# Performance work log

Hardware: AMD Instinct MI355X
Metric: run time of the kernel (lower is better)

Reference implementation:

```python
import jax, jax.numpy as jnp
import numpy as np

N = 100000
E = 3200000
IN_DIM = 128
HID = 64
BN_EPS = 1e-5


def _gcn_conv(x, W, b, src, dst, dinv):
    h = x @ W                                      # [N, out]
    coeff = (dinv[src] * dinv[dst])[:, None]       # [E, 1]
    msg = h[src] * coeff                           # gather over edges
    agg = jax.ops.segment_sum(msg, dst, num_segments=N)
    agg = agg + h * (dinv * dinv)[:, None]         # self-loop term
    return agg + b


def setup_inputs() -> dict:
    key = jax.random.key(0)
    ks = jax.random.split(key, 12)
    x = jax.random.normal(ks[0], (N, IN_DIM), dtype=jnp.float32)
    edge_index = jax.random.randint(ks[1], (2, E), 0, N, dtype=jnp.int64)
    s1 = 1.0 / np.sqrt(IN_DIM)
    s2 = 1.0 / np.sqrt(HID)
    W1 = jax.random.uniform(ks[2], (IN_DIM, HID), jnp.float32, -s1, s1)
    b1 = jnp.zeros((HID,), jnp.float32)
    W2 = jax.random.uniform(ks[3], (HID, HID), jnp.float32, -s2, s2)
    b2 = jnp.zeros((HID,), jnp.float32)
    W3 = jax.random.uniform(ks[4], (HID, 1), jnp.float32, -s2, s2)
    b3 = jnp.zeros((1,), jnp.float32)
    g1 = jnp.ones((HID,), jnp.float32)
    beta1 = jnp.zeros((HID,), jnp.float32)
    m1 = 0.1 * jax.random.normal(ks[5], (HID,), jnp.float32)
    v1 = jax.random.uniform(ks[6], (HID,), jnp.float32) + 0.5
    g2 = jnp.ones((HID,), jnp.float32)
    beta2 = jnp.zeros((HID,), jnp.float32)
    m2 = 0.1 * jax.random.normal(ks[7], (HID,), jnp.float32)
    v2 = jax.random.uniform(ks[8], (HID,), jnp.float32) + 0.5
    return {"x": x, "edge_index": edge_index,
            "W1": W1, "b1": b1, "W2": W2, "b2": b2, "W3": W3, "b3": b3,
            "g1": g1, "beta1": beta1, "m1": m1, "v1": v1,
            "g2": g2, "beta2": beta2, "m2": m2, "v2": v2}


def reference(x, edge_index, W1, b1, W2, b2, W3, b3,
              g1, beta1, m1, v1, g2, beta2, m2, v2):
    src, dst = edge_index[0], edge_index[1]
    # degree with self-loops (computed on destination index, PyG convention)
    deg = jax.ops.segment_sum(jnp.ones((E,), jnp.float32), dst, num_segments=N) + 1.0
    dinv = jax.lax.rsqrt(deg)

    def bn(h, g, beta, m, v):
        return (h - m) * jax.lax.rsqrt(v + BN_EPS) * g + beta

    h = _gcn_conv(x, W1, b1, src, dst, dinv)
    h = jax.nn.relu(bn(h, g1, beta1, m1, v1))  # dropout is a no-op in eval
    h = _gcn_conv(h, W2, b2, src, dst, dinv)
    h = jax.nn.relu(bn(h, g2, beta2, m2, v2))
    h = _gcn_conv(h, W3, b3, src, dst, dinv)
    return jax.nn.sigmoid(h)  # [N, 1]
```

## Files before the change

kernel.cpp:

```cpp
#include <hip/hip_runtime.h>
#include <math.h>

#define N_NODES 100000
#define E_EDGES 3200000
#define IN_DIM_ 128
#define HID_ 64
#define BN_EPS_ 1e-5f

#define PB 200
#define CHUNK 16000
#define NBUCK 391

typedef __attribute__((ext_vector_type(8))) short short8;
typedef __attribute__((ext_vector_type(4))) float f32x4;

__device__ inline ushort f2bf(float f) {
    union { float f; unsigned u; } c; c.f = f;
    unsigned r = c.u + 0x7fff + ((c.u >> 16) & 1);
    return (ushort)(r >> 16);
}
__device__ inline float bf_lo(unsigned p) { union { unsigned u; float f; } c; c.u = p << 16; return c.f; }
__device__ inline float bf_hi(unsigned p) { union { unsigned u; float f; } c; c.u = p & 0xffff0000u; return c.f; }

__global__ __launch_bounds__(256) void passA1_hist(const int* __restrict__ ei,
                                                   int* __restrict__ histPB) {
    __shared__ int hist[NBUCK];
    int t = threadIdx.x, b = blockIdx.x;
    for (int k = t; k < NBUCK; k += 256) hist[k] = 0;
    __syncthreads();
    int e0 = b * CHUNK, e1 = e0 + CHUNK;
    for (int e = e0 + t; e < e1; e += 256) {
        int d = ei[E_EDGES + e];
        atomicAdd(&hist[d >> 8], 1);
    }
    __syncthreads();
    for (int k = t; k < NBUCK; k += 256) histPB[k * PB + b] = hist[k];
}

__global__ __launch_bounds__(256) void scan_rows(int* __restrict__ histPB,
                                                 int* __restrict__ bucket_tot) {
    __shared__ int wsum[4];
    int k = blockIdx.x, t = threadIdx.x, lane = t & 63, wv = t >> 6;
    int v = (t < PB) ? histPB[k * PB + t] : 0;
    int s = v;
#pragma unroll
    for (int off = 1; off < 64; off <<= 1) {
        int u = __shfl_up(s, off, 64);
        if (lane >= off) s += u;
    }
    if (lane == 63) wsum[wv] = s;
    __syncthreads();
    int wbase = 0;
    for (int w = 0; w < wv; w++) wbase += wsum[w];
    if (t < PB) histPB[k * PB + t] = wbase + s - v;
    if (t == 255) bucket_tot[k] = wbase + s;
}

__global__ __launch_bounds__(512) void scan_totals(const int* __restrict__ bucket_tot,
                                                   int* __restrict__ bucket_base,
                                                   int* __restrict__ row_ptr) {
    __shared__ int wsum[8];
    int t = threadIdx.x, lane = t & 63, wv = t >> 6;
    int v = (t < NBUCK) ? bucket_tot[t] : 0;
    int s = v;
#pragma unroll
    for (int off = 1; off < 64; off <<= 1) {
        int u = __shfl_up(s, off, 64);
        if (lane >= off) s += u;
    }
    if (lane == 63) wsum[wv] = s;
    __syncthreads();
    int wbase = 0;
    for (int w = 0; w < wv; w++) wbase += wsum[w];
    if (t < NBUCK) bucket_base[t] = wbase + s - v;
    if (t == 0) {
        bucket_base[NBUCK] = E_EDGES;
        row_ptr[N_NODES] = E_EDGES;
    }
}

__global__ __launch_bounds__(256) void passA2_scatter(const int* __restrict__ ei,
                                                      const int* __restrict__ histPB,
                                                      const int* __restrict__ bucket_base,
                                                      int* __restrict__ ebuf) {
    __shared__ int cur[NBUCK];
    int t = threadIdx.x, b = blockIdx.x;
    for (int k = t; k < NBUCK; k += 256) cur[k] = bucket_base[k] + histPB[k * PB + b];
    __syncthreads();
    int e0 = b * CHUNK, e1 = e0 + CHUNK;
    for (int e = e0 + t; e < e1; e += 256) {
        int s = ei[e];
        int d = ei[E_EDGES + e];
        int bk = d >> 8;
        int pos = atomicAdd(&cur[bk], 1);
        ebuf[pos] = s | ((d & 255) << 17);
    }
}

__global__ __launch_bounds__(256) void passB_place(const int* __restrict__ ebuf,
                                                   const int* __restrict__ bucket_base,
                                                   int* __restrict__ row_ptr,
                                                   int* __restrict__ csr_src,
                                                   float* __restrict__ dinv) {
    __shared__ int hist[256];
    __shared__ int wsum[4];
    int b = blockIdx.x, t = threadIdx.x, lane = t & 63, wv = t >> 6;
    int base = bucket_base[b], end = bucket_base[b + 1];
    hist[t] = 0;
    __syncthreads();
    for (int k = base + t; k < end; k += 256)
        atomicAdd(&hist[ebuf[k] >> 17], 1);
    __syncthreads();
    int v = hist[t];
    int s = v;
#pragma unroll
    for (int off = 1; off < 64; off <<= 1) {
        int u = __shfl_up(s, off, 64);
        if (lane >= off) s += u;
    }
    if (lane == 63) wsum[wv] = s;
    __syncthreads();
    int wbase = 0;
    for (int w = 0; w < wv; w++) wbase += wsum[w];
    int excl = wbase + s - v;
    int node = b * 256 + t;
    if (node < N_NODES) {
        row_ptr[node] = base + excl;
        dinv[node] = rsqrtf((float)v + 1.0f);
    }
    __syncthreads();
    hist[t] = excl;
    __syncthreads();
    for (int k = base + t; k < end; k += 256) {
        int pv = ebuf[k];
        int pos = atomicAdd(&hist[pv >> 17], 1);
        csr_src[base + pos] = pv & 0x1FFFF;
    }
}

template<int K, bool BF16IN>
__global__ __launch_bounds__(256) void gemm_bf16(const void* __restrict__ Xv,
                                                 const float* __restrict__ W,
                                                 const float* __restrict__ dinv,
                                                 ushort* __restrict__ hs) {
    constexpr int KP = K + 8;
    __shared__ ushort A_lds[64][KP];
    __shared__ ushort Wt_lds[64][KP];
    int t = threadIdx.x;
    long row0 = (long)blockIdx.x * 64;

    for (int i = t; i < K * 16; i += 256) {
        float4 w4 = ((const float4*)W)[i];
        int k = i >> 4, n = (i & 15) * 4;
        Wt_lds[n + 0][k] = f2bf(w4.x);
        Wt_lds[n + 1][k] = f2bf(w4.y);
        Wt_lds[n + 2][k] = f2bf(w4.z);
        Wt_lds[n + 3][k] = f2bf(w4.w);
    }
    if (BF16IN) {
        constexpr int K2 = K / 2;
        const unsigned* X = (const unsigned*)Xv;
        for (int i = t; i < 64 * K2; i += 256) {
            int r = i / K2, c = i % K2;
            unsigned val = 0;
            long row = row0 + r;
            if (row < N_NODES) val = X[row * K2 + c];
            *(unsigned*)&A_lds[r][c * 2] = val;
        }
    } else {
        constexpr int K4 = K / 4;
        const float* X = (const float*)Xv;
        for (int i = t; i < 64 * K4; i += 256) {
            int r = i / K4, c = i % K4;
            float4 val = make_float4(0.f, 0.f, 0.f, 0.f);
            long row = row0 + r;
            if (row < N_NODES) val = ((const float4*)X)[row * K4 + c];
            int cb = c * 4;
            A_lds[r][cb + 0] = f2bf(val.x);
            A_lds[r][cb + 1] = f2bf(val.y);
            A_lds[r][cb + 2] = f2bf(val.z);
            A_lds[r][cb + 3] = f2bf(val.w);
        }
    }
    __syncthreads();

    int w = t >> 6, l = t & 63;
    int m = l & 15, quad = l >> 4;
    f32x4 acc[4];
#pragma unroll
    for (int c = 0; c < 4; c++) acc[c] = (f32x4){0.f, 0.f, 0.f, 0.f};

#pragma unroll
    for (int ch = 0; ch < K / 32; ch++) {
        short8 a = *(const short8*)&A_lds[16 * w + m][32 * ch + 8 * quad];
#pragma unroll
        for (int c = 0; c < 4; c++) {
            short8 b = *(const short8*)&Wt_lds[16 * c + m][32 * ch + 8 * quad];
            acc[c] = __builtin_amdgcn_mfma_f32_16x16x32_bf16(a, b, acc[c], 0, 0, 0);
        }
    }

#pragma unroll
    for (int r = 0; r < 4; r++) {
        long node = row0 + 16 * w + quad * 4 + r;
        if (node < N_NODES) {
            float dv = dinv[node];
#pragma unroll
            for (int c = 0; c < 4; c++)
                hs[node * 64 + 16 * c + m] = f2bf(acc[c][r] * dv);
        }
    }
}

template<bool LAST>
__global__ __launch_bounds__(256) void gather_feat(const int* __restrict__ row_ptr,
                                                   const int* __restrict__ csr_src,
                                                   const ushort* __restrict__ hs,
                                                   const float* __restrict__ dinv,
                                                   const float* __restrict__ b,
                                                   const float* __restrict__ g,
                                                   const float* __restrict__ beta,
                                                   const float* __restrict__ m,
                                                   const float* __restrict__ v,
                                                   unsigned* __restrict__ y,
                                                   const float* __restrict__ W3,
                                                   float* __restrict__ hs3, int n) {
    int i = (blockIdx.x * 256 + threadIdx.x) >> 6;
    if (i >= n) return;
    int l = threadIdx.x & 63;
    int es = l >> 3, fg = l & 7;
    const uint4* H4 = (const uint4*)hs;

    float a0 = 0.f, a1 = 0.f, a2 = 0.f, a3 = 0.f;
    float a4 = 0.f, a5 = 0.f, a6 = 0.f, a7 = 0.f;

    if (es == 0) {
        uint4 p = H4[(long)i * 8 + fg];
        a0 += bf_lo(p.x); a1 += bf_hi(p.x);
        a2 += bf_lo(p.y); a3 += bf_hi(p.y);
        a4 += bf_lo(p.z); a5 += bf_hi(p.z);
        a6 += bf_lo(p.w); a7 += bf_hi(p.w);
    }

    int beg = row_ptr[i], end = row_ptr[i + 1];
    int k = beg;
    for (; k + 16 <= end; k += 16) {
        int sA = csr_src[k + es];
        int sB = csr_src[k + 8 + es];
        uint4 pA = H4[(long)sA * 8 + fg];
        uint4 pB = H4[(long)sB * 8 + fg];
        a0 += bf_lo(pA.x) + bf_lo(pB.x); a1 += bf_hi(pA.x) + bf_hi(pB.x);
        a2 += bf_lo(pA.y) + bf_lo(pB.y); a3 += bf_hi(pA.y) + bf_hi(pB.y);
        a4 += bf_lo(pA.z) + bf_lo(pB.z); a5 += bf_hi(pA.z) + bf_hi(pB.z);
        a6 += bf_lo(pA.w) + bf_lo(pB.w); a7 += bf_hi(pA.w) + bf_hi(pB.w);
    }
    for (; k + 8 <= end; k += 8) {
        int s = csr_src[k + es];
        uint4 p = H4[(long)s * 8 + fg];
        a0 += bf_lo(p.x); a1 += bf_hi(p.x);
        a2 += bf_lo(p.y); a3 += bf_hi(p.y);
        a4 += bf_lo(p.z); a5 += bf_hi(p.z);
        a6 += bf_lo(p.w); a7 += bf_hi(p.w);
    }
    int rem = end - k;
    if (es < rem) {
        int s = csr_src[k + es];
        uint4 p = H4[(long)s * 8 + fg];
        a0 += bf_lo(p.x); a1 += bf_hi(p.x);
        a2 += bf_lo(p.y); a3 += bf_hi(p.y);
        a4 += bf_lo(p.z); a5 += bf_hi(p.z);
        a6 += bf_lo(p.w); a7 += bf_hi(p.w);
    }

#pragma unroll
    for (int off = 8; off < 64; off <<= 1) {
        a0 += __shfl_xor(a0, off, 64);
        a1 += __shfl_xor(a1, off, 64);
        a2 += __shfl_xor(a2, off, 64);
        a3 += __shfl_xor(a3, off, 64);
        a4 += __shfl_xor(a4, off, 64);
        a5 += __shfl_xor(a5, off, 64);
        a6 += __shfl_xor(a6, off, 64);
        a7 += __shfl_xor(a7, off, 64);
    }

    float4 bb0 = ((const float4*)b)[fg * 2],    bb1 = ((const float4*)b)[fg * 2 + 1];
    float4 gg0 = ((const float4*)g)[fg * 2],    gg1 = ((const float4*)g)[fg * 2 + 1];
    float4 be0 = ((const float4*)beta)[fg * 2], be1 = ((const float4*)beta)[fg * 2 + 1];
    float4 mm0 = ((const float4*)m)[fg * 2],    mm1 = ((const float4*)m)[fg * 2 + 1];
    float4 vv0 = ((const float4*)v)[fg * 2],    vv1 = ((const float4*)v)[fg * 2 + 1];
    float di = dinv[i];
    float o0 = fmaxf((di * a0 + bb0.x - mm0.x) * (gg0.x * rsqrtf(vv0.x + BN_EPS_)) + be0.x, 0.f);
    float o1 = fmaxf((di * a1 + bb0.y - mm0.y) * (gg0.y * rsqrtf(vv0.y + BN_EPS_)) + be0.y, 0.f);
    float o2 = fmaxf((di * a2 + bb0.z - mm0.z) * (gg0.z * rsqrtf(vv0.z + BN_EPS_)) + be0.z, 0.f);
    float o3 = fmaxf((di * a3 + bb0.w - mm0.w) * (gg0.w * rsqrtf(vv0.w + BN_EPS_)) + be0.w, 0.f);
    float o4 = fmaxf((di * a4 + bb1.x - mm1.x) * (gg1.x * rsqrtf(vv1.x + BN_EPS_)) + be1.x, 0.f);
    float o5 = fmaxf((di * a5 + bb1.y - mm1.y) * (gg1.y * rsqrtf(vv1.y + BN_EPS_)) + be1.y, 0.f);
    float o6 = fmaxf((di * a6 + bb1.z - mm1.z) * (gg1.z * rsqrtf(vv1.z + BN_EPS_)) + be1.z, 0.f);
    float o7 = fmaxf((di * a7 + bb1.w - mm1.w) * (gg1.w * rsqrtf(vv1.w + BN_EPS_)) + be1.w, 0.f);

    if (LAST) {
        float4 w30 = ((const float4*)W3)[fg * 2], w31 = ((const float4*)W3)[fg * 2 + 1];
        float p = o0 * w30.x + o1 * w30.y + o2 * w30.z + o3 * w30.w +
                  o4 * w31.x + o5 * w31.y + o6 * w31.z + o7 * w31.w;
#pragma unroll
        for (int off = 1; off < 8; off <<= 1)
            p += __shfl_xor(p, off, 64);
        if (l == 0) hs3[i] = p * di;
    } else {
        if (es == 0) {
            uint4 pk;
            pk.x = (unsigned)f2bf(o0) | ((unsigned)f2bf(o1) << 16);
            pk.y = (unsigned)f2bf(o2) | ((unsigned)f2bf(o3) << 16);
            pk.z = (unsigned)f2bf(o4) | ((unsigned)f2bf(o5) << 16);
            pk.w = (unsigned)f2bf(o6) | ((unsigned)f2bf(o7) << 16);
            ((uint4*)y)[(long)i * 8 + fg] = pk;
        }
    }
}

__global__ __launch_bounds__(256) void gather3(const int* __restrict__ row_ptr,
                                               const int* __restrict__ csr_src,
                                               const float* __restrict__ hs3,
                                               const float* __restrict__ dinv,
                                               const float* __restrict__ b3,
                                               float* __restrict__ out, int n) {
    int i = blockIdx.x * 256 + threadIdx.x;
    if (i >= n) return;
    int beg = row_ptr[i], end = row_ptr[i + 1];
    float s0 = hs3[i], s1 = 0.f, s2 = 0.f, s3 = 0.f;
    float s4 = 0.f, s5 = 0.f, s6 = 0.f, s7 = 0.f;
    int k = beg;
    for (; k + 8 <= end; k += 8) {
        s0 += hs3[csr_src[k]];
        s1 += hs3[csr_src[k + 1]];
        s2 += hs3[csr_src[k + 2]];
        s3 += hs3[csr_src[k + 3]];
        s4 += hs3[csr_src[k + 4]];
        s5 += hs3[csr_src[k + 5]];
        s6 += hs3[csr_src[k + 6]];
        s7 += hs3[csr_src[k + 7]];
    }
    for (; k < end; k++) s0 += hs3[csr_src[k]];
    float z = dinv[i] * (((s0 + s1) + (s2 + s3)) + ((s4 + s5) + (s6 + s7))) + b3[0];
    out[i] = 1.f / (1.f + expf(-z));
}

extern "C" void kernel_launch(void* const* d_in, const int* in_sizes, int n_in,
                              void* d_out, int out_size, void* d_ws, size_t ws_size,
                              hipStream_t stream) {
    const int N = N_NODES;
    const int E = E_EDGES;

    const float* x   = (const float*)d_in[0];
    const int*   ei  = (const int*)d_in[1];
    const float* W1  = (const float*)d_in[2];
    const float* b1  = (const float*)d_in[3];
    const float* W2  = (const float*)d_in[4];
    const float* b2  = (const float*)d_in[5];
    const float* W3  = (const float*)d_in[6];
    const float* b3  = (const float*)d_in[7];
    const float* g1  = (const float*)d_in[8];
    const float* bt1 = (const float*)d_in[9];
    const float* m1  = (const float*)d_in[10];
    const float* v1  = (const float*)d_in[11];
    const float* g2  = (const float*)d_in[12];
    const float* bt2 = (const float*)d_in[13];
    const float* m2  = (const float*)d_in[14];
    const float* v2  = (const float*)d_in[15];
    float* out = (float*)d_out;

    int*    wsi         = (int*)d_ws;
    float*  dinv        = (float*)wsi;
    float*  hs3         = (float*)(wsi + (long)N);
    int*    row_ptr     = wsi + 2L * N;
    int*    histPB      = wsi + 3L * N + 16;
    int*    bucket_tot  = histPB + NBUCK * PB;
    int*    bucket_base = bucket_tot + 400;
    int*    csr_src     = bucket_base + 400;
    ushort* hsb         = (ushort*)(csr_src + (long)E);
    unsigned* yb        = (unsigned*)(csr_src + (long)E + 32L * N);
    int*    ebuf        = (int*)hsb;

    passA1_hist<<<PB, 256, 0, stream>>>(ei, histPB);
    scan_rows<<<NBUCK, 256, 0, stream>>>(histPB, bucket_tot);
    scan_totals<<<1, 512, 0, stream>>>(bucket_tot, bucket_base, row_ptr);
    passA2_scatter<<<PB, 256, 0, stream>>>(ei, histPB, bucket_base, ebuf);
    passB_place<<<NBUCK, 256, 0, stream>>>(ebuf, bucket_base, row_ptr, csr_src, dinv);

    gemm_bf16<IN_DIM_, false><<<(N + 63) / 64, 256, 0, stream>>>(x, W1, dinv, hsb);
    gather_feat<false><<<N / 4, 256, 0, stream>>>(row_ptr, csr_src, hsb, dinv,
                                                  b1, g1, bt1, m1, v1, yb, W3, hs3, N);
    gemm_bf16<HID_, true><<<(N + 63) / 64, 256, 0, stream>>>(yb, W2, dinv, hsb);
    gather_feat<true><<<N / 4, 256, 0, stream>>>(row_ptr, csr_src, hsb, dinv,
                                                 b2, g2, bt2, m2, v2, yb, W3, hs3, N);
    gather3<<<(N + 255) / 256, 256, 0, stream>>>(row_ptr, csr_src, hs3, dinv, b3, out, N);
}
```

Measured before the change: 432.1 us.

## Stage CSR bucket scatter through LDS to coalesce global writes

The edge scatter kernel now sorts each chunk's edges by bucket in shared memory (local histogram, scan, local placement) and then writes them to global memory in bucket-contiguous runs, instead of scattering each edge directly to a random global slot. The CSR placement kernel likewise builds each bucket's sorted source list in shared memory and writes it out linearly, falling back to direct global writes for buckets exceeding the shared buffer. This targets the uncoalesced random global writes of the CSR build, at the cost of large LDS footprints (about 96KB per block in the scatter kernel) that cut occupancy and add an extra pass over the edge destinations.

Result: no change. 430.8 us (-0.3%).

```diff
diff --git a/kernel.cpp b/kernel.cpp
--- a/kernel.cpp
+++ b/kernel.cpp
@@ -10,6 +10,7 @@
 #define PB 200
 #define CHUNK 16000
 #define NBUCK 391
+#define BMAX 9600
 
 typedef __attribute__((ext_vector_type(8))) short short8;
 typedef __attribute__((ext_vector_type(4))) float f32x4;
@@ -79,29 +80,61 @@
     }
 }
 
-__global__ __launch_bounds__(256) void passA2_scatter(const int* __restrict__ ei,
-                                                      const int* __restrict__ histPB,
-                                                      const int* __restrict__ bucket_base,
-                                                      int* __restrict__ ebuf) {
+__global__ __launch_bounds__(256) void passA2_sorted(const int* __restrict__ ei,
+                                                     const int* __restrict__ histPB,
+                                                     const int* __restrict__ bucket_base,
+                                                     int* __restrict__ ebuf) {
+    __shared__ int sorted[CHUNK];
+    __shared__ ushort bid[CHUNK];
     __shared__ int cur[NBUCK];
+    __shared__ int lbase[NBUCK];
     int t = threadIdx.x, b = blockIdx.x;
-    for (int k = t; k < NBUCK; k += 256) cur[k] = bucket_base[k] + histPB[k * PB + b];
-    __syncthreads();
-    int e0 = b * CHUNK, e1 = e0 + CHUNK;
-    for (int e = e0 + t; e < e1; e += 256) {
+    for (int k = t; k < NBUCK; k += 256) cur[k] = 0;
+    __syncthreads();
+    int e0 = b * CHUNK;
+    for (int e = e0 + t; e < e0 + CHUNK; e += 256)
+        atomicAdd(&cur[ei[E_EDGES + e] >> 8], 1);
+    __syncthreads();
+    if (t < 64) {
+        int run = 0;
+        for (int c0 = 0; c0 < NBUCK; c0 += 64) {
+            int idx = c0 + t;
+            int v = (idx < NBUCK) ? cur[idx] : 0;
+            int s = v;
+#pragma unroll
+            for (int off = 1; off < 64; off <<= 1) {
+                int u = __shfl_up(s, off, 64);
+                if (t >= off) s += u;
+            }
+            if (idx < NBUCK) lbase[idx] = run + s - v;
+            run += __shfl(s, 63, 64);
+        }
+    }
+    __syncthreads();
+    for (int k = t; k < NBUCK; k += 256) cur[k] = lbase[k];
+    __syncthreads();
+    for (int e = e0 + t; e < e0 + CHUNK; e += 256) {
         int s = ei[e];
         int d = ei[E_EDGES + e];
-        int bk = d >> 8;
-        int pos = atomicAdd(&cur[bk], 1);
-        ebuf[pos] = s | ((d & 255) << 17);
-    }
-}
-
-__global__ __launch_bounds__(256) void passB_place(const int* __restrict__ ebuf,
-                                                   const int* __restrict__ bucket_base,
-                                                   int* __restrict__ row_ptr,
-                                                   int* __restrict__ csr_src,
-                                                   float* __restrict__ dinv) {
+        int k = d >> 8;
+        int pos = atomicAdd(&cur[k], 1);
+        sorted[pos] = s | ((d & 255) << 17);
+        bid[pos] = (ushort)k;
+    }
+    __syncthreads();
+    for (int j = t; j < CHUNK; j += 256) {
+        int k = bid[j];
+        int dest = bucket_base[k] + histPB[k * PB + b] + (j - lbase[k]);
+        ebuf[dest] = sorted[j];
+    }
+}
+
+__global__ __launch_bounds__(256) void passB_sorted(const int* __restrict__ ebuf,
+                                                    const int* __restrict__ bucket_base,
+                                                    int* __restrict__ row_ptr,
+                                                    int* __restrict__ csr_src,
+                                                    float* __restrict__ dinv) {
+    __shared__ int sorted[BMAX];
     __shared__ int hist[256];
     __shared__ int wsum[4];
     int b = blockIdx.x, t = threadIdx.x, lane = t & 63, wv = t >> 6;
@@ -134,8 +167,14 @@
     for (int k = base + t; k < end; k += 256) {
         int pv = ebuf[k];
         int pos = atomicAdd(&hist[pv >> 17], 1);
-        csr_src[base + pos] = pv & 0x1FFFF;
-    }
+        if (pos < BMAX) sorted[pos] = pv;
+        else csr_src[base + pos] = pv & 0x1FFFF;
+    }
+    __syncthreads();
+    int cnt = end - base;
+    if (cnt > BMAX) cnt = BMAX;
+    for (int j = t; j < cnt; j += 256)
+        csr_src[base + j] = sorted[j] & 0x1FFFF;
 }
 
 template<int K, bool BF16IN>
@@ -385,8 +424,8 @@
     passA1_hist<<<PB, 256, 0, stream>>>(ei, histPB);
     scan_rows<<<NBUCK, 256, 0, stream>>>(histPB, bucket_tot);
     scan_totals<<<1, 512, 0, stream>>>(bucket_tot, bucket_base, row_ptr);
-    passA2_scatter<<<PB, 256, 0, stream>>>(ei, histPB, bucket_base, ebuf);
-    passB_place<<<NBUCK, 256, 0, stream>>>(ebuf, bucket_base, row_ptr, csr_src, dinv);
+    passA2_sorted<<<PB, 256, 0, stream>>>(ei, histPB, bucket_base, ebuf);
+    passB_sorted<<<NBUCK, 256, 0, stream>>>(ebuf, bucket_base, row_ptr, csr_src, dinv);
 
     gemm_bf16<IN_DIM_, false><<<(N + 63) / 64, 256, 0, stream>>>(x, W1, dinv, hsb);
     gather_feat<false><<<N / 4, 256, 0, stream>>>(row_ptr, csr_src, hsb, dinv,
```
